# Optimization experiments

Hardware: AMD Instinct MI355X
Metric: run time of the kernel (lower is better)

## Reference

```python
import jax, jax.numpy as jnp
import numpy as np

B, L, H, NH = 4, 2048, 2048, 16
HD = H // NH  # head_dim = 128


def setup_inputs() -> dict:
    key = jax.random.key(0)
    ks = jax.random.split(key, 5)
    x = jax.random.normal(ks[0], (B, L, H), dtype=jnp.float32)
    Wqkv = jax.random.normal(ks[1], (H, 3 * H), dtype=jnp.float32) * (1.0 / np.sqrt(H))
    bqkv = jnp.zeros((3 * H,), dtype=jnp.float32)
    Wfc2 = jax.random.normal(ks[2], (H, H), dtype=jnp.float32) * (1.0 / np.sqrt(H))
    bfc2 = jnp.zeros((H,), dtype=jnp.float32)
    # RoPE tables over the FULL hidden dim (as in the torch module)
    inv_freq = 1.0 / (10000.0 ** (jnp.arange(0, H, 2, dtype=jnp.float32) / H))  # [H/2]
    t = jnp.arange(L, dtype=jnp.float32)
    freqs = jnp.outer(t, inv_freq)  # [L, H/2]
    return {"x": x, "Wqkv": Wqkv, "bqkv": bqkv, "Wfc2": Wfc2, "bfc2": bfc2,
            "cos": jnp.cos(freqs), "sin": jnp.sin(freqs)}


def _apply_rotary(u, cos, sin):
    # u: [b, l, H]; rotate halves over full hidden dim
    l = u.shape[1]
    d = u.shape[-1] // 2
    u1, u2 = u[..., :d], u[..., d:]
    c, s = cos[:l], sin[:l]  # [l, d] broadcast over batch
    return jnp.concatenate([u1 * c + u2 * s, -u1 * s + u2 * c], axis=-1)


def reference(x, Wqkv, bqkv, Wfc2, bfc2, cos, sin):
    b, l, _ = x.shape
    qkv = x @ Wqkv + bqkv  # [b, l, 3H]
    q, k, v = jnp.split(qkv, 3, axis=-1)
    q = _apply_rotary(q, cos, sin)
    k = _apply_rotary(k, cos, sin)
    # NOTE: heads are the FASTEST axis in the original view(b, l, head_dim, heads)
    def to_heads(u):
        return jnp.transpose(u.reshape(b, l, HD, NH), (0, 3, 1, 2))  # [b, h, l, d]
    q, k, v = to_heads(q), to_heads(k), to_heads(v)
    scale = 1.0 / np.sqrt(HD)
    scores = jnp.einsum('bhqd,bhkd->bhqk', q, k) * scale
    causal = jnp.tril(jnp.ones((l, l), dtype=bool))
    scores = jnp.where(causal, scores, jnp.finfo(scores.dtype).min)
    p = jax.nn.softmax(scores, axis=-1)
    y = jnp.einsum('bhqk,bhkd->bhqd', p, v)
    y = jnp.transpose(y, (0, 2, 1, 3)).reshape(b, l, H)  # [b, l, h*d]
    return jax.nn.silu(y @ Wfc2 + bfc2)
```

## Files before the change

### kernel.cpp

```cpp
#include <hip/hip_runtime.h>
#include <hip/hip_bf16.h>
#include <cstdint>
#include <cstddef>


typedef __attribute__((ext_vector_type(4))) float f32x4;
typedef __attribute__((ext_vector_type(8))) short bf16x8;
typedef __hip_bfloat16 bf16;

#define ASYNC16(lds, g)                                                                  \
  __builtin_amdgcn_global_load_lds((const __attribute__((address_space(1))) void*)(g),   \
                                   (__attribute__((address_space(3))) void*)(lds), 16, 0, 0)

__device__ __forceinline__ float b2f(bf16 v) { return __bfloat162float(v); }
__device__ __forceinline__ bf16 f2b(float v) { return __float2bfloat16(v); }
__device__ __forceinline__ short f2bs(float f) {
  bf16 h = __float2bfloat16(f);
  return __builtin_bit_cast(short, h);
}
__device__ __forceinline__ bf16x8 pack8(f32x4 a, f32x4 b) {
  bf16x8 r;
#pragma unroll
  for (int t = 0; t < 4; ++t) r[t] = f2bs(a[t]);
#pragma unroll
  for (int t = 0; t < 4; ++t) r[4 + t] = f2bs(b[t]);
  return r;
}

__global__ void conv_bf16(const float* __restrict__ src, bf16* __restrict__ dst) {
  size_t i = ((size_t)blockIdx.x * 256 + threadIdx.x) * 8;
  f32x4 a0 = *(const f32x4*)(src + i);
  f32x4 a1 = *(const f32x4*)(src + i + 4);
  *(bf16x8*)(dst + i) = pack8(a0, a1);
}

__global__ void transpose_conv(const float* __restrict__ src, bf16* __restrict__ dst,
                               int R, int C, int perm) {
  __shared__ float tile[32][33];
  int bx = blockIdx.x * 32, by = blockIdx.y * 32;
  int tx = threadIdx.x, ty = threadIdx.y;
  for (int i = ty; i < 32; i += 8) tile[i][tx] = src[(size_t)(by + i) * C + bx + tx];
  __syncthreads();
  for (int i = ty; i < 32; i += 8) {
    int c = bx + i;
    if (perm) {
      int cc = c & 2047;
      c = (c & ~2047) | (((cc & 15) << 7) | (cc >> 4));
    }
    dst[(size_t)c * R + by + tx] = f2b(tile[tx][i]);
  }
}

__global__ __launch_bounds__(256) void gemm_qkv(const bf16* __restrict__ A,
                                                const bf16* __restrict__ Bt,
                                                const float* __restrict__ biasf,
                                                bf16* __restrict__ Qg, bf16* __restrict__ Kg,
                                                bf16* __restrict__ Vg) {
  __shared__ alignas(16) bf16 smem[2 * 128 * 64];
  bf16* As = smem;
  bf16* Bs = smem + 128 * 64;
  const int K_ = 2048;
  int tid = threadIdx.x, lane = tid & 63, w = tid >> 6;
  int lr = lane & 15, hi = lane >> 4;
  int wm = (w >> 1) * 64, wn = (w & 1) * 64;
  int m0 = blockIdx.y * 128, n0 = blockIdx.x * 128;
  f32x4 acc[4][4];
#pragma unroll
  for (int im = 0; im < 4; ++im)
#pragma unroll
    for (int in = 0; in < 4; ++in) acc[im][in] = (f32x4){0.f, 0.f, 0.f, 0.f};

  for (int k0 = 0; k0 < K_; k0 += 64) {
    __syncthreads();
#pragma unroll
    for (int i = 0; i < 4; ++i) {
      int c = tid + 256 * i;
      int r = c >> 3, j = c & 7, jg = j ^ (r & 7);
      ASYNC16((char*)As + c * 16, (const char*)(A + (size_t)(m0 + r) * K_ + k0 + jg * 8));
    }
#pragma unroll
    for (int i = 0; i < 4; ++i) {
      int c = tid + 256 * i;
      int r = c >> 3, j = c & 7, jg = j ^ (r & 7);
      ASYNC16((char*)Bs + c * 16, (const char*)(Bt + (size_t)(n0 + r) * K_ + k0 + jg * 8));
    }
    __syncthreads();

#pragma unroll
    for (int ks = 0; ks < 2; ++ks) {
      bf16x8 afr[4], bfr[4];
#pragma unroll
      for (int im = 0; im < 4; ++im) {
        int r = wm + 16 * im + lr;
        afr[im] = *(const bf16x8*)((const char*)As + r * 128 + (((ks * 4 + hi) ^ (r & 7)) * 16));
      }
#pragma unroll
      for (int in = 0; in < 4; ++in) {
        int r = wn + 16 * in + lr;
        bfr[in] = *(const bf16x8*)((const char*)Bs + r * 128 + (((ks * 4 + hi) ^ (r & 7)) * 16));
      }
#pragma unroll
      for (int im = 0; im < 4; ++im)
#pragma unroll
        for (int in = 0; in < 4; ++in)
          acc[im][in] =
              __builtin_amdgcn_mfma_f32_16x16x32_bf16(afr[im], bfr[in], acc[im][in], 0, 0, 0);
    }
  }

  int which = n0 >> 11;
  int h = (n0 >> 7) & 15;
  int bq = m0 >> 11;
  int l_base = m0 & 2047;
  int bh = bq * 16 + h;
  float bv[4];
#pragma unroll
  for (int in = 0; in < 4; ++in)
    bv[in] = biasf[(which << 11) + ((wn + 16 * in + lr) << 4) + h];

  if (which < 2) {
    bf16* __restrict__ G = (which == 0) ? Qg : Kg;
#pragma unroll
    for (int im = 0; im < 4; ++im) {
#pragma unroll
      for (int in = 0; in < 4; ++in) {
        int d = wn + 16 * in + lr;
#pragma unroll
        for (int j = 0; j < 4; ++j) {
          int l = l_base + wm + 16 * im + 4 * hi + j;
          G[((size_t)bh * 2048 + l) * 128 + d] = f2b(acc[im][in][j] + bv[in]);
        }
      }
    }
  } else {
    __syncthreads();
#pragma unroll
    for (int im = 0; im < 4; ++im)
#pragma unroll
      for (int in = 0; in < 4; ++in) {
        int d = wn + 16 * in + lr;
#pragma unroll
        for (int j = 0; j < 4; ++j) {
          int l = wm + 16 * im + 4 * hi + j;
          int slot = (l >> 3) ^ (d & 15);
          smem[d * 128 + slot * 8 + (l & 7)] = f2b(acc[im][in][j] + bv[in]);
        }
      }
    __syncthreads();
#pragma unroll
    for (int s = 0; s < 8; ++s) {
      int d = (tid >> 4) + 16 * s;
      int lc = tid & 15;
      int slot = lc ^ (d & 15);
      bf16x8 v = *(const bf16x8*)(smem + d * 128 + slot * 8);
      *(bf16x8*)(Vg + ((size_t)bh * 128 + d) * 2048 + l_base + lc * 8) = v;
    }
  }
}

__global__ __launch_bounds__(256) void gemm_fc2(const bf16* __restrict__ A,
                                                const bf16* __restrict__ Bt,
                                                const float* __restrict__ biasf,
                                                float* __restrict__ Out) {
  __shared__ alignas(16) bf16 As[128 * 64];
  __shared__ alignas(16) bf16 Bs[128 * 64];
  const int K_ = 2048;
  int tid = threadIdx.x, lane = tid & 63, w = tid >> 6;
  int lr = lane & 15, hi = lane >> 4;
  int wm = (w >> 1) * 64, wn = (w & 1) * 64;
  int m0 = blockIdx.y * 128, n0 = blockIdx.x * 128;
  f32x4 acc[4][4];
#pragma unroll
  for (int im = 0; im < 4; ++im)
#pragma unroll
    for (int in = 0; in < 4; ++in) acc[im][in] = (f32x4){0.f, 0.f, 0.f, 0.f};

  for (int k0 = 0; k0 < K_; k0 += 64) {
    __syncthreads();
#pragma unroll
    for (int i = 0; i < 4; ++i) {
      int c = tid + 256 * i;
      int r = c >> 3, j = c & 7, jg = j ^ (r & 7);
      ASYNC16((char*)As + c * 16, (const char*)(A + (size_t)(m0 + r) * K_ + k0 + jg * 8));
    }
#pragma unroll
    for (int i = 0; i < 4; ++i) {
      int c = tid + 256 * i;
      int r = c >> 3, j = c & 7, jg = j ^ (r & 7);
      ASYNC16((char*)Bs + c * 16, (const char*)(Bt + (size_t)(n0 + r) * K_ + k0 + jg * 8));
    }
    __syncthreads();
#pragma unroll
    for (int ks = 0; ks < 2; ++ks) {
      bf16x8 afr[4], bfr[4];
#pragma unroll
      for (int im = 0; im < 4; ++im) {
        int r = wm + 16 * im + lr;
        afr[im] = *(const bf16x8*)((const char*)As + r * 128 + (((ks * 4 + hi) ^ (r & 7)) * 16));
      }
#pragma unroll
      for (int in = 0; in < 4; ++in) {
        int r = wn + 16 * in + lr;
        bfr[in] = *(const bf16x8*)((const char*)Bs + r * 128 + (((ks * 4 + hi) ^ (r & 7)) * 16));
      }
#pragma unroll
      for (int im = 0; im < 4; ++im)
#pragma unroll
        for (int in = 0; in < 4; ++in)
          acc[im][in] =
              __builtin_amdgcn_mfma_f32_16x16x32_bf16(afr[im], bfr[in], acc[im][in], 0, 0, 0);
    }
  }

#pragma unroll
  for (int im = 0; im < 4; ++im) {
#pragma unroll
    for (int in = 0; in < 4; ++in) {
      int c = n0 + wn + 16 * in + lr;
      float bv = biasf[c];
#pragma unroll
      for (int j = 0; j < 4; ++j) {
        int m = m0 + wm + 16 * im + 4 * hi + j;
        float z = acc[im][in][j] + bv;
        Out[(size_t)m * 2048 + c] = z / (1.f + __expf(-z));
      }
    }
  }
}

__global__ void rotary_kernel(bf16* __restrict__ Qg, bf16* __restrict__ Kg,
                              const float* __restrict__ cosp, const float* __restrict__ sinp) {
  int idx = blockIdx.x * 256 + threadIdx.x;
  int d = idx & 63;
  int l = (idx >> 6) & 2047;
  int bh = idx >> 17;
  int h = bh & 15;
  size_t base = ((size_t)bh * 2048 + l) * 128;
  int ang = l * 1024 + d * 16 + h;
  float c = cosp[ang], s = sinp[ang];
  float q1 = b2f(Qg[base + d]), q2 = b2f(Qg[base + d + 64]);
  Qg[base + d] = f2b(q1 * c + q2 * s);
  Qg[base + d + 64] = f2b(-q1 * s + q2 * c);
  float k1 = b2f(Kg[base + d]), k2 = b2f(Kg[base + d + 64]);
  Kg[base + d] = f2b(k1 * c + k2 * s);
  Kg[base + d + 64] = f2b(-k1 * s + k2 * c);
}

__global__ __launch_bounds__(256) void flash_kernel(const bf16* __restrict__ Qg,
                                                    const bf16* __restrict__ Kg,
                                                    const bf16* __restrict__ Vg,
                                                    bf16* __restrict__ Y) {
  __shared__ alignas(16) bf16 Qs[64 * 128];
  __shared__ alignas(16) bf16 Ks[64 * 128];
  __shared__ alignas(16) bf16 Vt[128 * 64];
  __shared__ alignas(16) bf16 Ps[4 * 16 * 72];
  int tid = threadIdx.x, lane = tid & 63, w = tid >> 6;
  int lr = lane & 15, hi = lane >> 4;
  int it = 31 - (int)blockIdx.x;
  int bh = blockIdx.y;
  int b = bh >> 4, h = bh & 15;
  int q0 = it * 64;
  const bf16* Qb = Qg + (size_t)bh * 2048 * 128;
  const bf16* Kb = Kg + (size_t)bh * 2048 * 128;
  const bf16* Vb = Vg + (size_t)bh * 128 * 2048;
  const float NEG = -1.0e30f;

#pragma unroll
  for (int i = 0; i < 4; ++i) {
    int c = tid + 256 * i;
    int r = c >> 4, j = c & 15, jg = j ^ (r & 7);
    ASYNC16((char*)Qs + c * 16, (const char*)(Qb + (size_t)(q0 + r) * 128 + jg * 8));
  }

  f32x4 o[8];
#pragma unroll
  for (int i = 0; i < 8; ++i) o[i] = (f32x4){0.f, 0.f, 0.f, 0.f};
  float m_i[4], l_i[4];
#pragma unroll
  for (int j = 0; j < 4; ++j) { m_i[j] = NEG; l_i[j] = 0.f; }
  const float scale = 0.08838834764831845f;

  for (int jt = 0; jt <= it; ++jt) {
    int k0 = jt * 64;
    __syncthreads();
#pragma unroll
    for (int i = 0; i < 4; ++i) {
      int c = tid + 256 * i;
      int r = c >> 4, j = c & 15, jg = j ^ (r & 7);
      ASYNC16((char*)Ks + c * 16, (const char*)(Kb + (size_t)(k0 + r) * 128 + jg * 8));
    }
#pragma unroll
    for (int i = 0; i < 4; ++i) {
      int c = tid + 256 * i;
      int r = c >> 3, j = c & 7, jg = j ^ (r & 7);
      ASYNC16((char*)Vt + c * 16, (const char*)(Vb + (size_t)r * 2048 + k0 + jg * 8));
    }
    __syncthreads();

    f32x4 sacc[4];
#pragma unroll
    for (int in = 0; in < 4; ++in) sacc[in] = (f32x4){0.f, 0.f, 0.f, 0.f};
#pragma unroll
    for (int ks = 0; ks < 4; ++ks) {
      int ar = 16 * w + lr;
      bf16x8 a = *(const bf16x8*)((const char*)Qs + ar * 256 + (((ks * 4 + hi) ^ (ar & 7)) * 16));
#pragma unroll
      for (int in = 0; in < 4; ++in) {
        int br = 16 * in + lr;
        bf16x8 bb =
            *(const bf16x8*)((const char*)Ks + br * 256 + (((ks * 4 + hi) ^ (br & 7)) * 16));
        sacc[in] = __builtin_amdgcn_mfma_f32_16x16x32_bf16(a, bb, sacc[in], 0, 0, 0);
      }
    }

    bool diag = (jt == it);
#pragma unroll
    for (int j = 0; j < 4; ++j) {
      float mx = NEG;
#pragma unroll
      for (int in = 0; in < 4; ++in) {
        float s = sacc[in][j] * scale;
        if (diag) {
          int qg = 16 * w + 4 * hi + j;
          int kg = 16 * in + lr;
          if (kg > qg) s = NEG;
        }
        sacc[in][j] = s;
        mx = fmaxf(mx, s);
      }
#pragma unroll
      for (int off = 1; off < 16; off <<= 1) mx = fmaxf(mx, __shfl_xor(mx, off));
      float mnew = fmaxf(m_i[j], mx);
      float alpha = __expf(m_i[j] - mnew);
      float rs = 0.f;
#pragma unroll
      for (int in = 0; in < 4; ++in) {
        float p = __expf(sacc[in][j] - mnew);
        sacc[in][j] = p;
        rs += p;
      }
#pragma unroll
      for (int off = 1; off < 16; off <<= 1) rs += __shfl_xor(rs, off);
      l_i[j] = alpha * l_i[j] + rs;
      m_i[j] = mnew;
#pragma unroll
      for (int inp = 0; inp < 8; ++inp) o[inp][j] *= alpha;
    }

#pragma unroll
    for (int j = 0; j < 4; ++j)
#pragma unroll
      for (int in = 0; in < 4; ++in)
        Ps[w * 1152 + (4 * hi + j) * 72 + 16 * in + lr] = f2b(sacc[in][j]);
    __syncthreads();

#pragma unroll
    for (int ko = 0; ko < 2; ++ko) {
      bf16x8 a = *(const bf16x8*)((const char*)Ps + (w * 1152 + lr * 72 + ko * 32 + hi * 8) * 2);
#pragma unroll
      for (int inp = 0; inp < 8; ++inp) {
        int br = 16 * inp + lr;
        bf16x8 bb =
            *(const bf16x8*)((const char*)Vt + br * 128 + (((ko * 4 + hi) ^ (br & 7)) * 16));
        o[inp] = __builtin_amdgcn_mfma_f32_16x16x32_bf16(a, bb, o[inp], 0, 0, 0);
      }
    }
  }

#pragma unroll
  for (int j = 0; j < 4; ++j) {
    int qg = q0 + 16 * w + 4 * hi + j;
    float inv = 1.f / l_i[j];
    size_t rowb = ((size_t)(b * 2048 + qg)) * 2048 + h * 128;
#pragma unroll
    for (int inp = 0; inp < 8; ++inp) {
      int dd = 16 * inp + lr;
      Y[rowb + dd] = f2b(o[inp][j] * inv);
    }
  }
}

extern "C" void kernel_launch(void* const* d_in, const int* in_sizes, int n_in,
                              void* d_out, int out_size, void* d_ws, size_t ws_size,
                              hipStream_t stream) {
  const float* x    = (const float*)d_in[0];
  const float* Wqkv = (const float*)d_in[1];
  const float* bqkv = (const float*)d_in[2];
  const float* Wfc2 = (const float*)d_in[3];
  const float* bfc2 = (const float*)d_in[4];
  const float* cosp = (const float*)d_in[5];
  const float* sinp = (const float*)d_in[6];
  float* out = (float*)d_out;

  bf16* ws = (bf16*)d_ws;
  bf16* Yg    = ws;
  bf16* WqkvT = ws;
  bf16* Qg    = ws + 16777216;
  bf16* Wfc2T = ws + 16777216;
  bf16* Kg    = ws + 33554432;
  bf16* Vg    = ws + 50331648;
  bf16* xb    = (bf16*)d_out;

  conv_bf16<<<8192, 256, 0, stream>>>(x, xb);
  transpose_conv<<<dim3(192, 64), dim3(32, 8), 0, stream>>>(Wqkv, WqkvT, 2048, 6144, 1);
  gemm_qkv<<<dim3(48, 64), 256, 0, stream>>>(xb, WqkvT, bqkv, Qg, Kg, Vg);
  rotary_kernel<<<32768, 256, 0, stream>>>(Qg, Kg, cosp, sinp);
  flash_kernel<<<dim3(32, 64), 256, 0, stream>>>(Qg, Kg, Vg, Yg);
  transpose_conv<<<dim3(64, 64), dim3(32, 8), 0, stream>>>(Wfc2, Wfc2T, 2048, 2048, 0);
  gemm_fc2<<<dim3(16, 64), 256, 0, stream>>>(Yg, Wfc2T, bfc2, out);
}
```

Before: 862.9 us.

## Hold Q fragments in registers and prefetch next K/V tile via registers

```diff
diff --git a/kernel.cpp b/kernel.cpp
--- a/kernel.cpp
+++ b/kernel.cpp
@@ -250,7 +250,6 @@
                                                     const bf16* __restrict__ Kg,
                                                     const bf16* __restrict__ Vg,
                                                     bf16* __restrict__ Y) {
-  __shared__ alignas(16) bf16 Qs[64 * 128];
   __shared__ alignas(16) bf16 Ks[64 * 128];
   __shared__ alignas(16) bf16 Vt[128 * 64];
   __shared__ alignas(16) bf16 Ps[4 * 16 * 72];
@@ -264,12 +263,21 @@
   const bf16* Kb = Kg + (size_t)bh * 2048 * 128;
   const bf16* Vb = Vg + (size_t)bh * 128 * 2048;
   const float NEG = -1.0e30f;
-
+  int ar = 16 * w + lr;
+
+  bf16x8 qf[4];
+#pragma unroll
+  for (int ks = 0; ks < 4; ++ks)
+    qf[ks] = *(const bf16x8*)(Qb + (size_t)(q0 + ar) * 128 + (ks * 4 + hi) * 8);
+
+  bf16x8 kreg[4], vreg[4];
 #pragma unroll
   for (int i = 0; i < 4; ++i) {
     int c = tid + 256 * i;
-    int r = c >> 4, j = c & 15, jg = j ^ (r & 7);
-    ASYNC16((char*)Qs + c * 16, (const char*)(Qb + (size_t)(q0 + r) * 128 + jg * 8));
+    int rk = c >> 4, jk = (c & 15) ^ (rk & 7);
+    kreg[i] = *(const bf16x8*)(Kb + (size_t)rk * 128 + jk * 8);
+    int rv = c >> 3, jv = (c & 7) ^ (rv & 7);
+    vreg[i] = *(const bf16x8*)(Vb + (size_t)rv * 2048 + jv * 8);
   }
 
   f32x4 o[8];
@@ -281,35 +289,38 @@
   const float scale = 0.08838834764831845f;
 
   for (int jt = 0; jt <= it; ++jt) {
-    int k0 = jt * 64;
     __syncthreads();
 #pragma unroll
     for (int i = 0; i < 4; ++i) {
       int c = tid + 256 * i;
-      int r = c >> 4, j = c & 15, jg = j ^ (r & 7);
-      ASYNC16((char*)Ks + c * 16, (const char*)(Kb + (size_t)(k0 + r) * 128 + jg * 8));
-    }
-#pragma unroll
-    for (int i = 0; i < 4; ++i) {
-      int c = tid + 256 * i;
-      int r = c >> 3, j = c & 7, jg = j ^ (r & 7);
-      ASYNC16((char*)Vt + c * 16, (const char*)(Vb + (size_t)r * 2048 + k0 + jg * 8));
-    }
-    __syncthreads();
+      *(bf16x8*)((char*)Ks + c * 16) = kreg[i];
+      *(bf16x8*)((char*)Vt + c * 16) = vreg[i];
+    }
+    __syncthreads();
+
+    if (jt < it) {
+      int k0n = (jt + 1) * 64;
+#pragma unroll
+      for (int i = 0; i < 4; ++i) {
+        int c = tid + 256 * i;
+        int rk = c >> 4, jk = (c & 15) ^ (rk & 7);
+        kreg[i] = *(const bf16x8*)(Kb + (size_t)(k0n + rk) * 128 + jk * 8);
+        int rv = c >> 3, jv = (c & 7) ^ (rv & 7);
+        vreg[i] = *(const bf16x8*)(Vb + (size_t)rv * 2048 + k0n + jv * 8);
+      }
+    }
 
     f32x4 sacc[4];
 #pragma unroll
     for (int in = 0; in < 4; ++in) sacc[in] = (f32x4){0.f, 0.f, 0.f, 0.f};
 #pragma unroll
     for (int ks = 0; ks < 4; ++ks) {
-      int ar = 16 * w + lr;
-      bf16x8 a = *(const bf16x8*)((const char*)Qs + ar * 256 + (((ks * 4 + hi) ^ (ar & 7)) * 16));
 #pragma unroll
       for (int in = 0; in < 4; ++in) {
         int br = 16 * in + lr;
         bf16x8 bb =
             *(const bf16x8*)((const char*)Ks + br * 256 + (((ks * 4 + hi) ^ (br & 7)) * 16));
-        sacc[in] = __builtin_amdgcn_mfma_f32_16x16x32_bf16(a, bb, sacc[in], 0, 0, 0);
+        sacc[in] = __builtin_amdgcn_mfma_f32_16x16x32_bf16(qf[ks], bb, sacc[in], 0, 0, 0);
       }
     }
 
@@ -352,7 +363,7 @@
 #pragma unroll
       for (int in = 0; in < 4; ++in)
         Ps[w * 1152 + (4 * hi + j) * 72 + 16 * in + lr] = f2b(sacc[in][j]);
-    __syncthreads();
+    asm volatile("s_waitcnt lgkmcnt(0)" ::: "memory");
 
 #pragma unroll
     for (int ko = 0; ko < 2; ++ko) {
```

Result: no change. 860.4 us (-0.3%).
